# Optimization experiments

Measured on AMD Instinct MI355X. Metric: run time of the kernel, lower is better.

The kernel has to match this reference:

```python
import jax, jax.numpy as jnp
import numpy as np

SEQ_LEN = 1024
CHANNELS = 64
UNITS = 32
WIDTH = 64
BATCH = 4
EPS = 1e-7


def setup_inputs() -> dict:
    key = jax.random.key(0)
    ks = jax.random.split(key, 5)
    x = jax.random.normal(ks[0], (BATCH, CHANNELS, SEQ_LEN), dtype=jnp.float32)
    Wt = jax.random.normal(ks[1], (UNITS, CHANNELS), dtype=jnp.float32) * (1.0 / np.sqrt(CHANNELS))
    Wx = jax.random.normal(ks[2], (UNITS, CHANNELS), dtype=jnp.float32) * (1.0 / np.sqrt(CHANNELS))
    Wa_w = jax.random.normal(ks[3], (1, UNITS), dtype=jnp.float32) * (1.0 / np.sqrt(UNITS))
    Wa_b = jnp.zeros((1,), dtype=jnp.float32)
    bh = jnp.zeros((UNITS,), dtype=jnp.float32)
    return {"x": x, "Wt": Wt, "Wx": Wx, "Wa_w": Wa_w, "Wa_b": Wa_b, "bh": bh}


def reference(x, Wt, Wx, Wa_w, Wa_b, bh):
    # x: (B, C, S) -> xt: (B, S, C)
    xt = jnp.transpose(x, (0, 2, 1))
    q = jnp.einsum('bsc,uc->bsu', xt, Wt)          # (B, S, U)
    k = jnp.einsum('bsc,uc->bsu', xt, Wx)          # (B, S, U)
    # additive (Bahdanau) scores: tanh over broadcast sum -> (B, S, S, U)
    h = jnp.tanh(q[:, :, None, :] + k[:, None, :, :] + bh)
    e = jnp.einsum('bstu,u->bst', h, Wa_w[0]) + Wa_b[0]   # (B, S, S)
    e = jnp.exp(e - jnp.max(e, axis=-1, keepdims=True))
    # local window mask: key index t allowed for query s iff s-W//2 <= t < s-W//2+W
    idx = jnp.arange(SEQ_LEN)
    lower = idx - WIDTH // 2                        # (S,)
    mask = (lower[:, None] <= idx[None, :]) & (idx[None, :] < (lower[:, None] + WIDTH))
    e = e * mask.astype(e.dtype)
    a = e / (jnp.sum(e, axis=-1, keepdims=True) + EPS)    # (B, S, S)
    v = jnp.einsum('bst,btc->bsc', a, xt)           # (B, S, C)
    v = jnp.transpose(v, (0, 2, 1))                 # (B, C, S)
    return (v, a)
```

## Files before the change

### kernel.cpp

```cpp
#include <hip/hip_runtime.h>
#include <cstddef>
#include <cmath>

#define SEQ    1024
#define CH     64
#define UNITS  32
#define WIDTH  64
#define HALFW  32
#define BATCH  4
#define EPS    1e-7f

#define TS     8
#define TT     72
#define XS     73
#define SCS    65

__global__ __launch_bounds__(256) void qk_kernel(
    const float* __restrict__ x, const float* __restrict__ Wt,
    const float* __restrict__ Wx, float* __restrict__ q, float* __restrict__ k)
{
    int bu = blockIdx.x;
    int u  = bu & (UNITS - 1);
    int b  = bu >> 5;
    int s4 = (int)threadIdx.x << 2;

    const float* wt = Wt + u * CH;
    const float* wx = Wx + u * CH;
    const float* xb = x + (size_t)b * CH * SEQ + s4;

    float4 qa = {0.f, 0.f, 0.f, 0.f};
    float4 ka = {0.f, 0.f, 0.f, 0.f};
#pragma unroll
    for (int c = 0; c < CH; ++c) {
        float4 xv = *reinterpret_cast<const float4*>(xb + (size_t)c * SEQ);
        float wtc = wt[c], wxc = wx[c];
        qa.x = fmaf(xv.x, wtc, qa.x); qa.y = fmaf(xv.y, wtc, qa.y);
        qa.z = fmaf(xv.z, wtc, qa.z); qa.w = fmaf(xv.w, wtc, qa.w);
        ka.x = fmaf(xv.x, wxc, ka.x); ka.y = fmaf(xv.y, wxc, ka.y);
        ka.z = fmaf(xv.z, wxc, ka.z); ka.w = fmaf(xv.w, wxc, ka.w);
    }
    size_t o = (size_t)bu * SEQ + s4;
    *reinterpret_cast<float4*>(q + o) = qa;
    *reinterpret_cast<float4*>(k + o) = ka;
}

__global__ __launch_bounds__(256) void attn_kernel(
    const float* __restrict__ x,
    const float* __restrict__ q, const float* __restrict__ k,
    const float* __restrict__ Wa_w, const float* __restrict__ Wa_b,
    const float* __restrict__ bh, float* __restrict__ out)
{
    __shared__ float xt[CH * XS];
    __shared__ float kt[UNITS * XS];
    __shared__ float qt[UNITS * TS];
    __shared__ float sc[TS * SCS];
    __shared__ float wa_s[UNITS], bh_s[UNITS];
    __shared__ float wab_s;

    int tid = threadIdx.x;
    int blk = blockIdx.x;
    int b   = blk >> 7;
    int s0  = (blk & 127) << 3;
    int t0  = s0 - HALFW;

    const float* xb = x + (size_t)b * CH * SEQ;
    const float* qb = q + (size_t)b * UNITS * SEQ;
    const float* kb = k + (size_t)b * UNITS * SEQ;

    {
        int u = tid >> 3, sl = tid & 7;
        qt[u * TS + sl] = qb[u * SEQ + s0 + sl];
    }
    if (tid < UNITS) { wa_s[tid] = Wa_w[tid]; bh_s[tid] = bh[tid]; }
    if (tid == 0)    { wab_s = Wa_b[0]; }
#pragma unroll
    for (int i = 0; i < 9; ++i) {
        int idx = i * 256 + tid;
        int u = idx / TT, tt = idx - u * TT;
        int t = t0 + tt; t = t < 0 ? 0 : (t >= SEQ ? SEQ - 1 : t);
        kt[u * XS + tt] = kb[u * SEQ + t];
    }
#pragma unroll
    for (int i = 0; i < 18; ++i) {
        int idx = i * 256 + tid;
        int c = idx / TT, tt = idx - c * TT;
        int t = t0 + tt; t = t < 0 ? 0 : (t >= SEQ ? SEQ - 1 : t);
        xt[c * XS + tt] = xb[c * SEQ + t];
    }
    __syncthreads();

    {
        int sl = tid >> 5, tlg = tid & 31;
        float e0 = wab_s, e1 = wab_s;
#pragma unroll
        for (int u = 0; u < UNITS; ++u) {
            float qv = qt[u * TS + sl] + bh_s[u];
            float k0 = kt[u * XS + sl + tlg];
            float k1 = kt[u * XS + sl + tlg + 32];
            float wa = wa_s[u];
            float z0 = qv + k0, z1 = qv + k1;
            float th0 = 1.f - 2.f * __builtin_amdgcn_rcpf(__expf(2.f * z0) + 1.f);
            float th1 = 1.f - 2.f * __builtin_amdgcn_rcpf(__expf(2.f * z1) + 1.f);
            e0 = fmaf(th0, wa, e0);
            e1 = fmaf(th1, wa, e1);
        }
        int ta = t0 + sl + tlg, tb = t0 + sl + tlg + 32;
        if (ta < 0 || ta >= SEQ) e0 = -INFINITY;
        if (tb < 0 || tb >= SEQ) e1 = -INFINITY;
        sc[sl * SCS + tlg]      = e0;
        sc[sl * SCS + tlg + 32] = e1;
    }
    __syncthreads();

    {
        int lane = tid & 63, wv = tid >> 6;
        int row  = wv * 2 + (lane >> 5);
        int l32  = lane & 31;
        float e0 = sc[row * SCS + l32];
        float e1 = sc[row * SCS + l32 + 32];
        float m = fmaxf(e0, e1);
#pragma unroll
        for (int off = 16; off >= 1; off >>= 1) m = fmaxf(m, __shfl_xor(m, off));
        float p0 = __expf(e0 - m), p1 = __expf(e1 - m);
        float ssum = p0 + p1;
#pragma unroll
        for (int off = 16; off >= 1; off >>= 1) ssum += __shfl_xor(ssum, off);
        float inv = __builtin_amdgcn_rcpf(ssum + EPS);
        sc[row * SCS + l32]      = p0 * inv;
        sc[row * SCS + l32 + 32] = p1 * inv;
    }
    __syncthreads();

    float* arow = out + (size_t)BATCH * CH * SEQ + ((size_t)(b * SEQ + s0)) * SEQ;
    int i0 = tid << 2;
#pragma unroll
    for (int r = 0; r < TS; ++r) {
        int lowerAbs = s0 + r - HALFW;
        int d = i0 - lowerAbs;
        float4 v4 = {0.f, 0.f, 0.f, 0.f};
        if (d > -4 && d < WIDTH) {
            const float* row = sc + r * SCS;
            if (d >= 0     && d     < WIDTH) v4.x = row[d];
            if (d + 1 >= 0 && d + 1 < WIDTH) v4.y = row[d + 1];
            if (d + 2 >= 0 && d + 2 < WIDTH) v4.z = row[d + 2];
            if (d + 3 >= 0 && d + 3 < WIDTH) v4.w = row[d + 3];
        }
        *reinterpret_cast<float4*>(arow + (size_t)r * SEQ + i0) = v4;
    }

    {
        int slv = tid & 7, c0 = (tid >> 3) << 1;
        float acc0 = 0.f, acc1 = 0.f;
        const float* x0 = xt + c0 * XS + slv;
        const float* x1 = x0 + XS;
        const float* ar = sc + slv * SCS;
#pragma unroll
        for (int j = 0; j < WIDTH; ++j) {
            float av = ar[j];
            acc0 = fmaf(av, x0[j], acc0);
            acc1 = fmaf(av, x1[j], acc1);
        }
        out[((size_t)(b * CH + c0)) * SEQ + s0 + slv]     = acc0;
        out[((size_t)(b * CH + c0 + 1)) * SEQ + s0 + slv] = acc1;
    }
}

extern "C" void kernel_launch(void* const* d_in, const int* in_sizes, int n_in,
                              void* d_out, int out_size, void* d_ws, size_t ws_size,
                              hipStream_t stream) {
    const float* x    = (const float*)d_in[0];
    const float* Wt   = (const float*)d_in[1];
    const float* Wx   = (const float*)d_in[2];
    const float* Wa_w = (const float*)d_in[3];
    const float* Wa_b = (const float*)d_in[4];
    const float* bh   = (const float*)d_in[5];
    float* out = (float*)d_out;

    float* q  = (float*)d_ws;
    float* kk = q + (size_t)BATCH * UNITS * SEQ;

    qk_kernel<<<BATCH * UNITS, 256, 0, stream>>>(x, Wt, Wx, q, kk);
    attn_kernel<<<BATCH * (SEQ / TS), 256, 0, stream>>>(x, q, kk, Wa_w, Wa_b, bh, out);
}
```

Before: 79.56 us.

## Transpose shared tiles to unit/channel-major, vectorize scores, split AV reduction across halves

Stores k, q and x tiles transposed in shared memory so score and AV loops can use float4 loads. The score and softmax phases are fused into one pass over 128 threads, each computing four keys, which drops one barrier. The AV product is split across two thread halves with a shared-memory reduction, and half the block writes the dense attention matrix while the other half reduces. The bias is folded into q in the first kernel. This adds staging buffers, a final transpose write and leaves half the threads idle during scoring.

```diff
diff --git a/kernel.cpp b/kernel.cpp
--- a/kernel.cpp
+++ b/kernel.cpp
@@ -11,13 +11,16 @@
 #define EPS    1e-7f
 
 #define TS     8
-#define TT     72
-#define XS     73
-#define SCS    65
+#define TT     80
+#define XTS    68
+#define KTS    36
+#define SCS    68
+#define VTS    68
 
 __global__ __launch_bounds__(256) void qk_kernel(
     const float* __restrict__ x, const float* __restrict__ Wt,
-    const float* __restrict__ Wx, float* __restrict__ q, float* __restrict__ k)
+    const float* __restrict__ Wx, const float* __restrict__ bh,
+    float* __restrict__ q, float* __restrict__ k)
 {
     int bu = blockIdx.x;
     int u  = bu & (UNITS - 1);
@@ -39,6 +42,8 @@
         ka.x = fmaf(xv.x, wxc, ka.x); ka.y = fmaf(xv.y, wxc, ka.y);
         ka.z = fmaf(xv.z, wxc, ka.z); ka.w = fmaf(xv.w, wxc, ka.w);
     }
+    float bv = bh[u];
+    qa.x += bv; qa.y += bv; qa.z += bv; qa.w += bv;
     size_t o = (size_t)bu * SEQ + s4;
     *reinterpret_cast<float4*>(q + o) = qa;
     *reinterpret_cast<float4*>(k + o) = ka;
@@ -46,15 +51,16 @@
 
 __global__ __launch_bounds__(256) void attn_kernel(
     const float* __restrict__ x,
-    const float* __restrict__ q, const float* __restrict__ k,
+    const float* __restrict__ qp, const float* __restrict__ k,
     const float* __restrict__ Wa_w, const float* __restrict__ Wa_b,
-    const float* __restrict__ bh, float* __restrict__ out)
+    float* __restrict__ out)
 {
-    __shared__ float xt[CH * XS];
-    __shared__ float kt[UNITS * XS];
-    __shared__ float qt[UNITS * TS];
-    __shared__ float sc[TS * SCS];
-    __shared__ float wa_s[UNITS], bh_s[UNITS];
+    __shared__ __align__(16) float xT[TT * XTS];
+    __shared__ __align__(16) float kT[TT * KTS];
+    __shared__ __align__(16) float qT[TS * KTS];
+    __shared__ __align__(16) float sc[TS * SCS];
+    __shared__ __align__(16) float vt[TS * VTS];
+    __shared__ __align__(16) float wa_s[UNITS];
     __shared__ float wab_s;
 
     int tid = threadIdx.x;
@@ -63,105 +69,149 @@
     int s0  = (blk & 127) << 3;
     int t0  = s0 - HALFW;
 
-    const float* xb = x + (size_t)b * CH * SEQ;
-    const float* qb = q + (size_t)b * UNITS * SEQ;
-    const float* kb = k + (size_t)b * UNITS * SEQ;
-
-    {
-        int u = tid >> 3, sl = tid & 7;
-        qt[u * TS + sl] = qb[u * SEQ + s0 + sl];
-    }
-    if (tid < UNITS) { wa_s[tid] = Wa_w[tid]; bh_s[tid] = bh[tid]; }
-    if (tid == 0)    { wab_s = Wa_b[0]; }
-#pragma unroll
-    for (int i = 0; i < 9; ++i) {
+    const float* xb = x  + (size_t)b * CH * SEQ;
+    const float* qb = qp + (size_t)b * UNITS * SEQ;
+    const float* kb = k  + (size_t)b * UNITS * SEQ;
+
+#pragma unroll
+    for (int i = 0; i < 5; ++i) {
         int idx = i * 256 + tid;
-        int u = idx / TT, tt = idx - u * TT;
-        int t = t0 + tt; t = t < 0 ? 0 : (t >= SEQ ? SEQ - 1 : t);
-        kt[u * XS + tt] = kb[u * SEQ + t];
-    }
-#pragma unroll
-    for (int i = 0; i < 18; ++i) {
+        int cg = idx / TT;
+        int tt = idx - cg * TT;
+        int t = t0 + tt; t = t < 0 ? 0 : (t > SEQ - 1 ? SEQ - 1 : t);
+        float4 v4;
+        v4.x = xb[(4 * cg + 0) * SEQ + t];
+        v4.y = xb[(4 * cg + 1) * SEQ + t];
+        v4.z = xb[(4 * cg + 2) * SEQ + t];
+        v4.w = xb[(4 * cg + 3) * SEQ + t];
+        *reinterpret_cast<float4*>(&xT[tt * XTS + 4 * cg]) = v4;
+    }
+#pragma unroll
+    for (int i = 0; i < 3; ++i) {
         int idx = i * 256 + tid;
-        int c = idx / TT, tt = idx - c * TT;
-        int t = t0 + tt; t = t < 0 ? 0 : (t >= SEQ ? SEQ - 1 : t);
-        xt[c * XS + tt] = xb[c * SEQ + t];
-    }
-    __syncthreads();
-
-    {
-        int sl = tid >> 5, tlg = tid & 31;
-        float e0 = wab_s, e1 = wab_s;
-#pragma unroll
-        for (int u = 0; u < UNITS; ++u) {
-            float qv = qt[u * TS + sl] + bh_s[u];
-            float k0 = kt[u * XS + sl + tlg];
-            float k1 = kt[u * XS + sl + tlg + 32];
-            float wa = wa_s[u];
-            float z0 = qv + k0, z1 = qv + k1;
-            float th0 = 1.f - 2.f * __builtin_amdgcn_rcpf(__expf(2.f * z0) + 1.f);
-            float th1 = 1.f - 2.f * __builtin_amdgcn_rcpf(__expf(2.f * z1) + 1.f);
-            e0 = fmaf(th0, wa, e0);
-            e1 = fmaf(th1, wa, e1);
+        if (idx < TT * (UNITS / 4)) {
+            int uq = idx / TT;
+            int tt = idx - uq * TT;
+            int t = t0 + tt; t = t < 0 ? 0 : (t > SEQ - 1 ? SEQ - 1 : t);
+            float4 v4;
+            v4.x = kb[(4 * uq + 0) * SEQ + t];
+            v4.y = kb[(4 * uq + 1) * SEQ + t];
+            v4.z = kb[(4 * uq + 2) * SEQ + t];
+            v4.w = kb[(4 * uq + 3) * SEQ + t];
+            *reinterpret_cast<float4*>(&kT[tt * KTS + 4 * uq]) = v4;
         }
-        int ta = t0 + sl + tlg, tb = t0 + sl + tlg + 32;
-        if (ta < 0 || ta >= SEQ) e0 = -INFINITY;
-        if (tb < 0 || tb >= SEQ) e1 = -INFINITY;
-        sc[sl * SCS + tlg]      = e0;
-        sc[sl * SCS + tlg + 32] = e1;
-    }
-    __syncthreads();
-
-    {
-        int lane = tid & 63, wv = tid >> 6;
-        int row  = wv * 2 + (lane >> 5);
-        int l32  = lane & 31;
-        float e0 = sc[row * SCS + l32];
-        float e1 = sc[row * SCS + l32 + 32];
-        float m = fmaxf(e0, e1);
-#pragma unroll
-        for (int off = 16; off >= 1; off >>= 1) m = fmaxf(m, __shfl_xor(m, off));
+    }
+    if (tid < 64) {
+        int sl = tid >> 3, uq = tid & 7;
+        float4 v4;
+        v4.x = qb[(4 * uq + 0) * SEQ + s0 + sl];
+        v4.y = qb[(4 * uq + 1) * SEQ + s0 + sl];
+        v4.z = qb[(4 * uq + 2) * SEQ + s0 + sl];
+        v4.w = qb[(4 * uq + 3) * SEQ + s0 + sl];
+        *reinterpret_cast<float4*>(&qT[sl * KTS + 4 * uq]) = v4;
+    }
+    if (tid < UNITS) wa_s[tid] = Wa_w[tid];
+    if (tid == 0)    wab_s = Wa_b[0];
+    __syncthreads();
+
+    if (tid < 128) {
+        int sl = tid >> 4, tq = tid & 15;
+        int j0 = 4 * tq;
+        float e0 = wab_s, e1 = wab_s, e2 = wab_s, e3 = wab_s;
+#pragma unroll
+        for (int uq = 0; uq < 8; ++uq) {
+            float4 q4 = *reinterpret_cast<const float4*>(&qT[sl * KTS + 4 * uq]);
+            float4 w4 = *reinterpret_cast<const float4*>(&wa_s[4 * uq]);
+#pragma unroll
+            for (int e = 0; e < 4; ++e) {
+                float4 k4 = *reinterpret_cast<const float4*>(
+                    &kT[(sl + j0 + e) * KTS + 4 * uq]);
+                float z0 = q4.x + k4.x, z1 = q4.y + k4.y;
+                float z2 = q4.z + k4.z, z3 = q4.w + k4.w;
+                float t0f = 1.f - 2.f * __builtin_amdgcn_rcpf(__expf(2.f * z0) + 1.f);
+                float t1f = 1.f - 2.f * __builtin_amdgcn_rcpf(__expf(2.f * z1) + 1.f);
+                float t2f = 1.f - 2.f * __builtin_amdgcn_rcpf(__expf(2.f * z2) + 1.f);
+                float t3f = 1.f - 2.f * __builtin_amdgcn_rcpf(__expf(2.f * z3) + 1.f);
+                float acc = fmaf(t0f, w4.x, fmaf(t1f, w4.y,
+                            fmaf(t2f, w4.z, t3f * w4.w)));
+                if      (e == 0) e0 += acc;
+                else if (e == 1) e1 += acc;
+                else if (e == 2) e2 += acc;
+                else             e3 += acc;
+            }
+        }
+        int tb = t0 + sl + j0;
+        if (tb + 0 < 0 || tb + 0 >= SEQ) e0 = -INFINITY;
+        if (tb + 1 < 0 || tb + 1 >= SEQ) e1 = -INFINITY;
+        if (tb + 2 < 0 || tb + 2 >= SEQ) e2 = -INFINITY;
+        if (tb + 3 < 0 || tb + 3 >= SEQ) e3 = -INFINITY;
+
+        float m = fmaxf(fmaxf(e0, e1), fmaxf(e2, e3));
+#pragma unroll
+        for (int off = 8; off >= 1; off >>= 1) m = fmaxf(m, __shfl_xor(m, off));
         float p0 = __expf(e0 - m), p1 = __expf(e1 - m);
-        float ssum = p0 + p1;
-#pragma unroll
-        for (int off = 16; off >= 1; off >>= 1) ssum += __shfl_xor(ssum, off);
+        float p2 = __expf(e2 - m), p3 = __expf(e3 - m);
+        float ssum = (p0 + p1) + (p2 + p3);
+#pragma unroll
+        for (int off = 8; off >= 1; off >>= 1) ssum += __shfl_xor(ssum, off);
         float inv = __builtin_amdgcn_rcpf(ssum + EPS);
-        sc[row * SCS + l32]      = p0 * inv;
-        sc[row * SCS + l32 + 32] = p1 * inv;
-    }
-    __syncthreads();
-
-    float* arow = out + (size_t)BATCH * CH * SEQ + ((size_t)(b * SEQ + s0)) * SEQ;
-    int i0 = tid << 2;
-#pragma unroll
-    for (int r = 0; r < TS; ++r) {
-        int lowerAbs = s0 + r - HALFW;
-        int d = i0 - lowerAbs;
-        float4 v4 = {0.f, 0.f, 0.f, 0.f};
-        if (d > -4 && d < WIDTH) {
-            const float* row = sc + r * SCS;
-            if (d >= 0     && d     < WIDTH) v4.x = row[d];
-            if (d + 1 >= 0 && d + 1 < WIDTH) v4.y = row[d + 1];
-            if (d + 2 >= 0 && d + 2 < WIDTH) v4.z = row[d + 2];
-            if (d + 3 >= 0 && d + 3 < WIDTH) v4.w = row[d + 3];
+        float4 a4 = {p0 * inv, p1 * inv, p2 * inv, p3 * inv};
+        *reinterpret_cast<float4*>(&sc[sl * SCS + j0]) = a4;
+    }
+    __syncthreads();
+
+    int jh  = tid >> 7;
+    int r   = tid & 127;
+    int slv = r >> 4;
+    int cg  = r & 15;
+    float4 acc = {0.f, 0.f, 0.f, 0.f};
+#pragma unroll 8
+    for (int jj = 0; jj < 32; ++jj) {
+        int j = jh * 32 + jj;
+        float a = sc[slv * SCS + j];
+        float4 x4 = *reinterpret_cast<const float4*>(
+            &xT[(slv + j) * XTS + 4 * cg]);
+        acc.x = fmaf(a, x4.x, acc.x);
+        acc.y = fmaf(a, x4.y, acc.y);
+        acc.z = fmaf(a, x4.z, acc.z);
+        acc.w = fmaf(a, x4.w, acc.w);
+    }
+    if (jh == 1)
+        *reinterpret_cast<float4*>(&vt[slv * VTS + 4 * cg]) = acc;
+    __syncthreads();
+
+    if (jh == 0) {
+        float4 p = *reinterpret_cast<const float4*>(&vt[slv * VTS + 4 * cg]);
+        acc.x += p.x; acc.y += p.y; acc.z += p.z; acc.w += p.w;
+        *reinterpret_cast<float4*>(&vt[slv * VTS + 4 * cg]) = acc;
+    } else {
+        float* abase = out + (size_t)BATCH * CH * SEQ
+                           + ((size_t)(b * SEQ + s0)) * SEQ;
+#pragma unroll
+        for (int i = 0; i < 16; ++i) {
+            int slot = i * 128 + r;
+            int row  = slot >> 8;
+            int i0   = (slot & 255) << 2;
+            int d = i0 - (s0 + row - HALFW);
+            float4 w4 = {0.f, 0.f, 0.f, 0.f};
+            if (d > -4 && d < WIDTH) {
+                const float* srow = &sc[row * SCS];
+                if (d >= 0     && d     < WIDTH) w4.x = srow[d];
+                if (d + 1 >= 0 && d + 1 < WIDTH) w4.y = srow[d + 1];
+                if (d + 2 >= 0 && d + 2 < WIDTH) w4.z = srow[d + 2];
+                if (d + 3 >= 0 && d + 3 < WIDTH) w4.w = srow[d + 3];
+            }
+            *reinterpret_cast<float4*>(&abase[(size_t)row * SEQ + i0]) = w4;
         }
-        *reinterpret_cast<float4*>(arow + (size_t)r * SEQ + i0) = v4;
-    }
-
-    {
-        int slv = tid & 7, c0 = (tid >> 3) << 1;
-        float acc0 = 0.f, acc1 = 0.f;
-        const float* x0 = xt + c0 * XS + slv;
-        const float* x1 = x0 + XS;
-        const float* ar = sc + slv * SCS;
-#pragma unroll
-        for (int j = 0; j < WIDTH; ++j) {
-            float av = ar[j];
-            acc0 = fmaf(av, x0[j], acc0);
-            acc1 = fmaf(av, x1[j], acc1);
-        }
-        out[((size_t)(b * CH + c0)) * SEQ + s0 + slv]     = acc0;
-        out[((size_t)(b * CH + c0 + 1)) * SEQ + s0 + slv] = acc1;
+    }
+    __syncthreads();
+
+    float* vbase = out + ((size_t)b * CH) * SEQ + s0;
+#pragma unroll
+    for (int i = 0; i < 2; ++i) {
+        int idx = i * 256 + tid;
+        int c = idx >> 3, sl2 = idx & 7;
+        vbase[(size_t)c * SEQ + sl2] = vt[sl2 * VTS + c];
     }
 }
 
@@ -179,6 +229,6 @@
     float* q  = (float*)d_ws;
     float* kk = q + (size_t)BATCH * UNITS * SEQ;
 
-    qk_kernel<<<BATCH * UNITS, 256, 0, stream>>>(x, Wt, Wx, q, kk);
-    attn_kernel<<<BATCH * (SEQ / TS), 256, 0, stream>>>(x, q, kk, Wa_w, Wa_b, bh, out);
+    qk_kernel<<<BATCH * UNITS, 256, 0, stream>>>(x, Wt, Wx, bh, q, kk);
+    attn_kernel<<<BATCH * (SEQ / TS), 256, 0, stream>>>(x, q, kk, Wa_w, Wa_b, out);
 }
```

New measurement: 83.69 us. 5.2% more time.
